# Optimization experiments

Measured on AMD Instinct MI355X. Metric: run time of the kernel, lower is better.

The kernel has to match this reference:

```python
import jax, jax.numpy as jnp
import numpy as np

K = 3            # kernel_size
FINAL = 112      # final_size
DIM = 256        # in_dim


def _blur_kernel():
    # arange(-2,3)^2 * (-1/sqrt(0.5)), exp, outer product, normalized
    f = np.exp((np.arange(-2, 3, dtype=np.float32) ** 2) * (-1.0 / np.sqrt(0.5)))
    k = np.outer(f, f)
    k /= k.sum()
    return jnp.asarray(k, dtype=jnp.float32)


def setup_inputs() -> dict:
    key = jax.random.key(0)
    k1, k2, k3, k4, k5 = jax.random.split(key, 5)
    hr_feats = jax.random.normal(k1, (4, DIM, 224, 224), dtype=jnp.float32)
    attn_kernel = jax.random.normal(k2, (K * K, DIM, K, K), dtype=jnp.float32) * 0.01 + 1.0
    kernel_bias = jax.random.normal(k3, (K * K,), dtype=jnp.float32) * 0.01
    logit_bias = jax.random.normal(k4, (1, K * K, 1, 1), dtype=jnp.float32) * 0.1
    keep_mask = jax.random.uniform(k5, (4, K * K, FINAL, FINAL)) > 0.2
    return {"hr_feats": hr_feats, "attn_kernel": attn_kernel,
            "kernel_bias": kernel_bias, "logit_bias": logit_bias,
            "keep_mask": keep_mask}


def reference(hr_feats, attn_kernel, kernel_bias, logit_bias, keep_mask):
    b, c, h, w = hr_feats.shape
    stride = h // FINAL
    pad = K // 2
    dn = ("NCHW", "OIHW", "NCHW")

    # depthwise 5x5 gaussian blur (blur_attn=True)
    blur_w = jnp.broadcast_to(_blur_kernel().reshape(1, 1, 5, 5), (c, 1, 5, 5))
    inputs = jax.lax.conv_general_dilated(
        hr_feats, blur_w, (1, 1), ((2, 2), (2, 2)),
        dimension_numbers=dn, feature_group_count=c)

    # attention logits: conv2d with k^2 output channels
    patches = jax.lax.conv_general_dilated(
        inputs, attn_kernel, (stride, stride), ((pad, pad), (pad, pad)),
        dimension_numbers=dn) + kernel_bias[None, :, None, None]

    logits = patches * keep_mask + logit_bias  # random keep mask + bias
    attn = jax.nn.softmax(logits, axis=1)       # over k^2 window positions

    # unfold: patches stacked as (c, kh, kw) in channel dim, matching F.unfold
    uf = jax.lax.conv_general_dilated_patches(
        inputs, (K, K), (stride, stride), ((pad, pad), (pad, pad)),
        dimension_numbers=dn)
    uf = uf.reshape(b, c, K * K, FINAL, FINAL)

    return jnp.einsum("bckhw,bkhw->bchw", uf, attn)
```

## Files before the change

### kernel.cpp

```cpp
#include <hip/hip_runtime.h>
#include <cmath>

#define FINAL 112
#define HW    224
#define DIM   256
#define HW2   (HW*HW)
#define F2    (FINAL*FINAL)

__device__ __forceinline__ void blur_weights(float fn[5]) {
    double fd[5]; double s = 0.0;
#pragma unroll
    for (int t = 0; t < 5; ++t) {
        double d = (double)(t - 2);
        fd[t] = exp(-1.4142135623730951 * d * d);
        s += fd[t];
    }
#pragma unroll
    for (int t = 0; t < 5; ++t) fn[t] = (float)(fd[t] / s);
}

__device__ __forceinline__ unsigned short f2bf(float x) {
    unsigned int u = __float_as_uint(x);
    return (unsigned short)((u + 0x7fffu + ((u >> 16) & 1u)) >> 16);
}
__device__ __forceinline__ unsigned int pack2(float a, float b) {
    return (unsigned int)f2bf(a) | ((unsigned int)f2bf(b) << 16);
}
__device__ __forceinline__ float bflo(unsigned int q) { return __uint_as_float(q << 16); }
__device__ __forceinline__ float bfhi(unsigned int q) { return __uint_as_float(q & 0xffff0000u); }

__device__ __forceinline__ float mask_val(const void* m, int flag, size_t idx) {
    if (flag == 0) return ((const int*)m)[idx] ? 1.0f : 0.0f;
    if (flag == 1) return ((const unsigned char*)m)[idx] ? 1.0f : 0.0f;
    if (flag == 2) return (((const float*)m)[idx] != 0.0f) ? 1.0f : 0.0f;
    return ((const long long*)m)[idx] ? 1.0f : 0.0f;
}

__global__ void k_detect(const unsigned int* __restrict__ m, int* __restrict__ flag, int nwords) {
    __shared__ int s_b123, s_3f, s_oddnz;
    if (threadIdx.x == 0) { s_b123 = 0; s_3f = 0; s_oddnz = 0; }
    __syncthreads();
    int b123 = 0, c3f = 0, oddnz = 0;
    for (int i = threadIdx.x; i < nwords; i += blockDim.x) {
        unsigned int u = m[i];
        if (u & 0xFFFFFF00u) b123++;
        if ((u >> 24) == 0x3Fu) c3f++;
        if ((i & 1) && u) oddnz++;
    }
    if (b123) atomicAdd(&s_b123, b123);
    if (c3f) atomicAdd(&s_3f, c3f);
    if (oddnz) atomicAdd(&s_oddnz, oddnz);
    __syncthreads();
    if (threadIdx.x == 0) {
        int f;
        if (s_b123 == 0) f = (s_oddnz == 0) ? 3 : 0;
        else if (s_3f > nwords / 8) f = 2;
        else f = 1;
        *flag = f;
    }
}


__device__ __forceinline__ float4 f4fma(float a, float4 x, float4 y) {
    return make_float4(fmaf(a, x.x, y.x), fmaf(a, x.y, y.y),
                       fmaf(a, x.z, y.z), fmaf(a, x.w, y.w));
}

__launch_bounds__(256)
__global__ void k_blur(const float* __restrict__ hr, unsigned short* __restrict__ blurh) {
    const int bc = blockIdx.x;
    const int w = threadIdx.x >> 6, lane = threadIdx.x & 63;
    const bool act = (lane < 56);
    float fn[5]; blur_weights(fn);
    const float4* src = (const float4*)(hr + (size_t)bc * HW2);
    unsigned short* dst = blurh + (size_t)bc * HW2;
    const int rbase = w * 56 - 2;

    float4 z = make_float4(0.f, 0.f, 0.f, 0.f);
    float4 w0 = z, w1 = z, w2 = z, w3 = z, w4 = z;

#pragma unroll
    for (int p = 0; p < 4; ++p) {
        const int g = rbase + p;
        float4 v = z;
        if (g >= 0 && g < HW && act) v = src[(size_t)g * 56 + lane];
        w0 = w1; w1 = w2; w2 = w3; w3 = w4; w4 = v;
    }

#pragma unroll 4
    for (int i = 4; i < 60; ++i) {
        const int g = rbase + i;
        float4 v = z;
        if (g < HW && act) v = src[(size_t)g * 56 + lane];
        w0 = w1; w1 = w2; w2 = w3; w3 = w4; w4 = v;

        float4 vb = z;
        vb = f4fma(fn[0], w0, vb);
        vb = f4fma(fn[1], w1, vb);
        vb = f4fma(fn[2], w2, vb);
        vb = f4fma(fn[3], w3, vb);
        vb = f4fma(fn[4], w4, vb);

        float lz = __shfl_up(vb.z, 1), lw = __shfl_up(vb.w, 1);
        if (lane == 0) { lz = 0.f; lw = 0.f; }
        float rx = __shfl_down(vb.x, 1), ry = __shfl_down(vb.y, 1);
        float win[8] = { lz, lw, vb.x, vb.y, vb.z, vb.w, rx, ry };
        float o[4];
#pragma unroll
        for (int j = 0; j < 4; ++j) {
            float s = 0.f;
#pragma unroll
            for (int t = 0; t < 5; ++t) s = fmaf(fn[t], win[j + t], s);
            o[j] = s;
        }
        if (act) {
            uint2 pk; pk.x = pack2(o[0], o[1]); pk.y = pack2(o[2], o[3]);
            *(uint2*)(dst + (size_t)(g - 2) * HW + 4 * lane) = pk;
        }
    }
}

__launch_bounds__(256)
__global__ void k_logits_part(const unsigned short* __restrict__ blurh,
                              const float* __restrict__ wk, float* __restrict__ part) {
    const int cg  = blockIdx.x & 15;
    const int rst = blockIdx.x >> 4;
    const int oyq = rst % 28, b = rst / 28;
    const int w = threadIdx.x >> 6, lane = threadIdx.x & 63;
    const int oy = oyq * 4 + w;
    const bool act = (lane < 56);
    const int row0 = 2 * oy - 1;

    float accE[9], accO[9];
#pragma unroll
    for (int o = 0; o < 9; ++o) { accE[o] = 0.f; accO[o] = 0.f; }

#pragma unroll 4
    for (int k = 0; k < 16; ++k) {
        const int c = cg * 16 + k;
        const unsigned short* base = blurh + ((size_t)(b * DIM + c)) * HW2;
        float tE[3][3], tO[3][3];
#pragma unroll
        for (int kh = 0; kh < 3; ++kh) {
            const int row = row0 + kh;
            uint2 q = make_uint2(0u, 0u);
            if (row >= 0 && act)
                q = *(const uint2*)(base + (size_t)row * HW + 4 * lane);
            float vx = bflo(q.x), vy = bfhi(q.x), vz = bflo(q.y), vw = bfhi(q.y);
            float pv = __shfl_up(vw, 1);
            if (lane == 0) pv = 0.f;
            tE[kh][0] = pv; tE[kh][1] = vx; tE[kh][2] = vy;
            tO[kh][0] = vy; tO[kh][1] = vz; tO[kh][2] = vw;
        }
        const float* wc = wk + (size_t)c * 9;
#pragma unroll
        for (int o = 0; o < 9; ++o) {
            const float* wo = wc + (size_t)o * (DIM * 9);
#pragma unroll
            for (int kh = 0; kh < 3; ++kh)
#pragma unroll
                for (int j = 0; j < 3; ++j) {
                    const float wvv = wo[kh * 3 + j];
                    accE[o] = fmaf(wvv, tE[kh][j], accE[o]);
                    accO[o] = fmaf(wvv, tO[kh][j], accO[o]);
                }
        }
    }
    if (act) {
        float* pb = part + (((size_t)(cg * 4 + b)) * 9) * F2 + (size_t)oy * FINAL;
#pragma unroll
        for (int o = 0; o < 9; ++o)
            *(float2*)(pb + (size_t)o * F2 + 2 * lane) = make_float2(accE[o], accO[o]);
    }
}

__launch_bounds__(256)
__global__ void k_softmax(const float* __restrict__ part, const float* __restrict__ kb,
                          const float* __restrict__ lb, const void* __restrict__ mask,
                          float* __restrict__ attn) {
    __shared__ int sb, sf, so;
    if (threadIdx.x == 0) { sb = 0; sf = 0; so = 0; }
    __syncthreads();
    const unsigned int* mw = (const unsigned int*)mask;
    int b123 = 0, c3f = 0, oddnz = 0;
    for (int i = threadIdx.x; i < 2048; i += 256) {
        unsigned int u = mw[i];
        if (u & 0xFFFFFF00u) b123++;
        if ((u >> 24) == 0x3Fu) c3f++;
        if ((i & 1) && u) oddnz++;
    }
    if (b123) atomicAdd(&sb, b123);
    if (c3f) atomicAdd(&sf, c3f);
    if (oddnz) atomicAdd(&so, oddnz);
    __syncthreads();
    int flag;
    if (sb == 0) flag = (so == 0) ? 3 : 0;
    else if (sf > 256) flag = 2;
    else flag = 1;

    const int idx = blockIdx.x * 256 + threadIdx.x;
    const int b = idx / F2, p = idx - b * F2;
    float l[9]; float mx = -3.4e38f;
#pragma unroll
    for (int o = 0; o < 9; ++o) {
        float s = 0.f;
#pragma unroll
        for (int g = 0; g < 16; ++g)
            s += part[(((size_t)(g * 4 + b)) * 9 + o) * F2 + p];
        size_t midx = ((size_t)b * 9 + o) * F2 + p;
        float lo = (s + kb[o]) * mask_val(mask, flag, midx) + lb[o];
        l[o] = lo; mx = fmaxf(mx, lo);
    }
    float sum = 0.f;
#pragma unroll
    for (int o = 0; o < 9; ++o) { l[o] = expf(l[o] - mx); sum += l[o]; }
    const float inv = 1.0f / sum;
#pragma unroll
    for (int o = 0; o < 9; ++o)
        attn[((size_t)b * 9 + o) * F2 + p] = l[o] * inv;
}

__launch_bounds__(256)
__global__ void k_out(const unsigned short* __restrict__ blurh,
                      const float* __restrict__ attn, float* __restrict__ out) {
    const int cg  = blockIdx.x & 7;
    const int rst = blockIdx.x >> 3;
    const int oy = rst % FINAL, b = rst / FINAL;
    const int w = threadIdx.x >> 6, lane = threadIdx.x & 63;
    const bool act = (lane < 56);
    const int row0 = 2 * oy - 1;

    __shared__ float sa[9][FINAL];
    for (int i = threadIdx.x; i < 9 * FINAL; i += 256) {
        int o = i / FINAL, x = i - o * FINAL;
        sa[o][x] = attn[((size_t)b * 9 + o) * F2 + (size_t)oy * FINAL + x];
    }
    __syncthreads();

    float aE[9], aO[9];
#pragma unroll
    for (int o = 0; o < 9; ++o) {
        float2 a = act ? *(const float2*)&sa[o][2 * lane] : make_float2(0.f, 0.f);
        aE[o] = a.x; aO[o] = a.y;
    }
#pragma unroll 4
    for (int k = 0; k < 8; ++k) {
        const int c = (cg << 5) + (w << 3) + k;
        const unsigned short* base = blurh + ((size_t)(b * DIM + c)) * HW2;
        float oE = 0.f, oO = 0.f;
#pragma unroll
        for (int kh = 0; kh < 3; ++kh) {
            const int row = row0 + kh;
            uint2 q = make_uint2(0u, 0u);
            if (row >= 0 && act)
                q = *(const uint2*)(base + (size_t)row * HW + 4 * lane);
            float vx = bflo(q.x), vy = bfhi(q.x), vz = bflo(q.y), vw = bfhi(q.y);
            float pv = __shfl_up(vw, 1);
            if (lane == 0) pv = 0.f;
            oE = fmaf(aE[kh * 3 + 0], pv, oE);
            oE = fmaf(aE[kh * 3 + 1], vx, oE);
            oE = fmaf(aE[kh * 3 + 2], vy, oE);
            oO = fmaf(aO[kh * 3 + 0], vy, oO);
            oO = fmaf(aO[kh * 3 + 1], vz, oO);
            oO = fmaf(aO[kh * 3 + 2], vw, oO);
        }
        if (act)
            *(float2*)(out + ((size_t)(b * DIM + c)) * F2 + (size_t)oy * FINAL + 2 * lane)
                = make_float2(oE, oO);
    }
}


__launch_bounds__(512, 1)
__global__ void k_logits_fb(const float* __restrict__ hr, const float* __restrict__ wk,
                            const float* __restrict__ kb, const float* __restrict__ lb,
                            const void* __restrict__ mask, const int* __restrict__ flagp,
                            float* __restrict__ attn) {
    const int blk = blockIdx.x;
    const int b = blk / FINAL, oy = blk % FINAL;
    const int tid = threadIdx.x;
    const int half = tid >> 8;
    const int lane = tid & 255;
    __shared__ float sIn[2][7][HW];
    __shared__ float sV[2][3][HW + 4];
    __shared__ float sB[2][3][HW + 2];
    __shared__ float sW[2][81];
    __shared__ float sL[1008];
    float fn[5]; blur_weights(fn);
    if (lane < 3) {
        sV[half][lane][0] = 0.f; sV[half][lane][1] = 0.f;
        sV[half][lane][HW + 2] = 0.f; sV[half][lane][HW + 3] = 0.f;
        sB[half][lane][0] = 0.f; sB[half][lane][HW + 1] = 0.f;
    }
    float acc0 = 0.f, acc1 = 0.f;
    const int s1 = tid + 512;
    const int o0 = tid / FINAL, x0 = tid % FINAL;
    const int o1 = s1 / FINAL, x1 = s1 % FINAL;
    const bool has1 = (s1 < 9 * FINAL);
    for (int c0 = 0; c0 < DIM; c0 += 2) {
        const int c = c0 + half;
        const float* src = hr + ((size_t)(b * DIM + c)) * HW2;
        for (int i = lane; i < 7 * HW; i += 256) {
            int r = i / HW, x = i - r * HW;
            int g = 2 * oy - 3 + r;
            sIn[half][r][x] = (g >= 0 && g < HW) ? src[(size_t)g * HW + x] : 0.f;
        }
        if (lane < 81) {
            int o = lane / 9, kk = lane - o * 9;
            sW[half][lane] = wk[((size_t)(o * DIM + c)) * 9 + kk];
        }
        __syncthreads();
        if (lane < HW) {
#pragma unroll
            for (int j = 0; j < 3; ++j) {
                int by = 2 * oy - 1 + j;
                float v = 0.f;
#pragma unroll
                for (int t = 0; t < 5; ++t) v = fmaf(fn[t], sIn[half][j + t][lane], v);
                sV[half][j][lane + 2] = (by >= 0 && by < HW) ? v : 0.f;
            }
        }
        __syncthreads();
        if (lane < HW) {
#pragma unroll
            for (int j = 0; j < 3; ++j) {
                float v = 0.f;
#pragma unroll
                for (int t = 0; t < 5; ++t) v = fmaf(fn[t], sV[half][j][lane + t], v);
                sB[half][j][lane + 1] = v;
            }
        }
        __syncthreads();
#pragma unroll
        for (int cc = 0; cc < 2; ++cc) {
            const float* w = sW[cc];
            float a0 = 0.f;
#pragma unroll
            for (int kh = 0; kh < 3; ++kh)
#pragma unroll
                for (int kw = 0; kw < 3; ++kw)
                    a0 = fmaf(sB[cc][kh][2 * x0 + kw], w[o0 * 9 + kh * 3 + kw], a0);
            acc0 += a0;
            if (has1) {
                float a1v = 0.f;
#pragma unroll
                for (int kh = 0; kh < 3; ++kh)
#pragma unroll
                    for (int kw = 0; kw < 3; ++kw)
                        a1v = fmaf(sB[cc][kh][2 * x1 + kw], w[o1 * 9 + kh * 3 + kw], a1v);
                acc1 += a1v;
            }
        }
        __syncthreads();
    }
    sL[tid] = acc0;
    if (has1) sL[s1] = acc1;
    __syncthreads();
    if (tid < FINAL) {
        const int flag = *flagp;
        float l[9]; float mx = -3.4e38f;
#pragma unroll
        for (int o = 0; o < 9; ++o) {
            size_t midx = (((size_t)b * 9 + o) * FINAL + oy) * FINAL + tid;
            float patch = sL[o * FINAL + tid] + kb[o];
            float lo = patch * mask_val(mask, flag, midx) + lb[o];
            l[o] = lo;
            mx = fmaxf(mx, lo);
        }
        float sum = 0.f;
#pragma unroll
        for (int o = 0; o < 9; ++o) { l[o] = expf(l[o] - mx); sum += l[o]; }
        float inv = 1.0f / sum;
#pragma unroll
        for (int o = 0; o < 9; ++o)
            attn[(((size_t)b * 9 + o) * FINAL + oy) * FINAL + tid] = l[o] * inv;
    }
}

__launch_bounds__(512, 1)
__global__ void k_out_fb(const float* __restrict__ hr, const float* __restrict__ attn,
                         float* __restrict__ out) {
    const int blk = blockIdx.x;
    const int b = blk / FINAL, oy = blk % FINAL;
    const int tid = threadIdx.x;
    const int half = tid >> 8;
    const int lane = tid & 255;
    __shared__ float sIn[2][7][HW];
    __shared__ float sV[2][3][HW + 4];
    __shared__ float sB[2][3][HW + 2];
    __shared__ float sA[9][FINAL];
    float fn[5]; blur_weights(fn);
    if (lane < 3) {
        sV[half][lane][0] = 0.f; sV[half][lane][1] = 0.f;
        sV[half][lane][HW + 2] = 0.f; sV[half][lane][HW + 3] = 0.f;
        sB[half][lane][0] = 0.f; sB[half][lane][HW + 1] = 0.f;
    }
    for (int i = tid; i < 9 * FINAL; i += 512) {
        int o = i / FINAL, x = i - o * FINAL;
        sA[o][x] = attn[(((size_t)b * 9 + o) * FINAL + oy) * FINAL + x];
    }
    for (int c0 = 0; c0 < DIM; c0 += 2) {
        const int c = c0 + half;
        const float* src = hr + ((size_t)(b * DIM + c)) * HW2;
        for (int i = lane; i < 7 * HW; i += 256) {
            int r = i / HW, x = i - r * HW;
            int g = 2 * oy - 3 + r;
            sIn[half][r][x] = (g >= 0 && g < HW) ? src[(size_t)g * HW + x] : 0.f;
        }
        __syncthreads();
        if (lane < HW) {
#pragma unroll
            for (int j = 0; j < 3; ++j) {
                int by = 2 * oy - 1 + j;
                float v = 0.f;
#pragma unroll
                for (int t = 0; t < 5; ++t) v = fmaf(fn[t], sIn[half][j + t][lane], v);
                sV[half][j][lane + 2] = (by >= 0 && by < HW) ? v : 0.f;
            }
        }
        __syncthreads();
        if (lane < HW) {
#pragma unroll
            for (int j = 0; j < 3; ++j) {
                float v = 0.f;
#pragma unroll
                for (int t = 0; t < 5; ++t) v = fmaf(fn[t], sV[half][j][lane + t], v);
                sB[half][j][lane + 1] = v;
            }
        }
        __syncthreads();
        if (lane < FINAL) {
            float a = 0.f;
#pragma unroll
            for (int kh = 0; kh < 3; ++kh)
#pragma unroll
                for (int kw = 0; kw < 3; ++kw)
                    a = fmaf(sA[kh * 3 + kw][lane], sB[half][kh][2 * lane + kw], a);
            out[(((size_t)(b * DIM + c)) * FINAL + oy) * FINAL + lane] = a;
        }
    }
}

extern "C" void kernel_launch(void* const* d_in, const int* in_sizes, int n_in,
                              void* d_out, int out_size, void* d_ws, size_t ws_size,
                              hipStream_t stream) {
    const float* hr   = (const float*)d_in[0];
    const float* wk   = (const float*)d_in[1];
    const float* kb   = (const float*)d_in[2];
    const float* lb   = (const float*)d_in[3];
    const void*  mask = d_in[4];
    float* out = (float*)d_out;

    const size_t ATTN_B = (size_t)4 * 9 * F2 * 4;
    const size_t PART_B = ATTN_B * 16;
    const size_t BLUR_B = (size_t)4 * DIM * HW2 * 2;
    int*   flag = (int*)d_ws;
    float* attn = (float*)((char*)d_ws + 256);
    float* part = (float*)((char*)d_ws + 256 + ATTN_B);
    unsigned short* blurh = (unsigned short*)((char*)d_ws + 256 + ATTN_B + PART_B);
    const size_t need = 256 + ATTN_B + PART_B + BLUR_B;

    if (ws_size >= need) {
        k_blur<<<4 * DIM, 256, 0, stream>>>(hr, blurh);
        k_logits_part<<<4 * 28 * 16, 256, 0, stream>>>(blurh, wk, part);
        k_softmax<<<(4 * F2) / 256, 256, 0, stream>>>(part, kb, lb, mask, attn);
        k_out<<<4 * FINAL * 8, 256, 0, stream>>>(blurh, attn, out);
    } else {
        k_detect<<<1, 1024, 0, stream>>>((const unsigned int*)mask, flag, (4 * 9 * F2) / 4);
        k_logits_fb<<<4 * FINAL, 512, 0, stream>>>(hr, wk, kb, lb, mask, flag, attn);
        k_out_fb<<<4 * FINAL, 512, 0, stream>>>(hr, attn, out);
    }
}
```

Before: 187.3 us.

## Reuse overlapping rows across two output rows, stage weights in LDS, use hardware bf16 pack

k_out now computes two output rows per block. It loads 5 input rows instead of 3 per row, so the shared middle row is read once for both outputs, and the grid is halved. k_logits_part stages its 16-channel slice of the attention weights in shared memory instead of reading them from global memory inside the inner loop, and lowers the unroll factor. The blur kernel replaces the software bf16 rounding with the v_cvt_pk_bf16_f32 instruction, which depends on that instruction existing on the target and rounding the same way. The extra registers in k_out may reduce occupancy.

```diff
diff --git a/kernel.cpp b/kernel.cpp
--- a/kernel.cpp
+++ b/kernel.cpp
@@ -19,12 +19,10 @@
     for (int t = 0; t < 5; ++t) fn[t] = (float)(fd[t] / s);
 }
 
-__device__ __forceinline__ unsigned short f2bf(float x) {
-    unsigned int u = __float_as_uint(x);
-    return (unsigned short)((u + 0x7fffu + ((u >> 16) & 1u)) >> 16);
-}
-__device__ __forceinline__ unsigned int pack2(float a, float b) {
-    return (unsigned int)f2bf(a) | ((unsigned int)f2bf(b) << 16);
+__device__ __forceinline__ unsigned int cvt_pk_bf16(float a, float b) {
+    unsigned int r;
+    asm("v_cvt_pk_bf16_f32 %0, %1, %2" : "=v"(r) : "v"(a), "v"(b));
+    return r;
 }
 __device__ __forceinline__ float bflo(unsigned int q) { return __uint_as_float(q << 16); }
 __device__ __forceinline__ float bfhi(unsigned int q) { return __uint_as_float(q & 0xffff0000u); }
@@ -114,7 +112,7 @@
             o[j] = s;
         }
         if (act) {
-            uint2 pk; pk.x = pack2(o[0], o[1]); pk.y = pack2(o[2], o[3]);
+            uint2 pk; pk.x = cvt_pk_bf16(o[0], o[1]); pk.y = cvt_pk_bf16(o[2], o[3]);
             *(uint2*)(dst + (size_t)(g - 2) * HW + 4 * lane) = pk;
         }
     }
@@ -131,11 +129,18 @@
     const bool act = (lane < 56);
     const int row0 = 2 * oy - 1;
 
+    __shared__ float sw[9][16][9];
+    for (int i = threadIdx.x; i < 1296; i += 256) {
+        const int o = i / 144, r = i - o * 144;
+        sw[o][r / 9][r % 9] = wk[((size_t)o * DIM + cg * 16) * 9 + r];
+    }
+    __syncthreads();
+
     float accE[9], accO[9];
 #pragma unroll
     for (int o = 0; o < 9; ++o) { accE[o] = 0.f; accO[o] = 0.f; }
 
-#pragma unroll 4
+#pragma unroll 2
     for (int k = 0; k < 16; ++k) {
         const int c = cg * 16 + k;
         const unsigned short* base = blurh + ((size_t)(b * DIM + c)) * HW2;
@@ -152,10 +157,9 @@
             tE[kh][0] = pv; tE[kh][1] = vx; tE[kh][2] = vy;
             tO[kh][0] = vy; tO[kh][1] = vz; tO[kh][2] = vw;
         }
-        const float* wc = wk + (size_t)c * 9;
 #pragma unroll
         for (int o = 0; o < 9; ++o) {
-            const float* wo = wc + (size_t)o * (DIM * 9);
+            const float* wo = sw[o][k];
 #pragma unroll
             for (int kh = 0; kh < 3; ++kh)
 #pragma unroll
@@ -225,48 +229,61 @@
                       const float* __restrict__ attn, float* __restrict__ out) {
     const int cg  = blockIdx.x & 7;
     const int rst = blockIdx.x >> 3;
-    const int oy = rst % FINAL, b = rst / FINAL;
+    const int yq = rst % 56, b = rst / 56;
+    const int oy0 = 2 * yq;
     const int w = threadIdx.x >> 6, lane = threadIdx.x & 63;
     const bool act = (lane < 56);
-    const int row0 = 2 * oy - 1;
-
-    __shared__ float sa[9][FINAL];
-    for (int i = threadIdx.x; i < 9 * FINAL; i += 256) {
-        int o = i / FINAL, x = i - o * FINAL;
-        sa[o][x] = attn[((size_t)b * 9 + o) * F2 + (size_t)oy * FINAL + x];
-    }
-    __syncthreads();
-
-    float aE[9], aO[9];
-#pragma unroll
-    for (int o = 0; o < 9; ++o) {
-        float2 a = act ? *(const float2*)&sa[o][2 * lane] : make_float2(0.f, 0.f);
-        aE[o] = a.x; aO[o] = a.y;
-    }
-#pragma unroll 4
+    const int rbase = 2 * oy0 - 1;
+
+    __shared__ float sa[9][2][FINAL];
+    for (int i = threadIdx.x; i < 9 * 2 * FINAL; i += 256) {
+        const int o = i / (2 * FINAL), r = i - o * 2 * FINAL;
+        const int y = r / FINAL, x = r - y * FINAL;
+        sa[o][y][x] = attn[((size_t)b * 9 + o) * F2 + (size_t)(oy0 + y) * FINAL + x];
+    }
+    __syncthreads();
+
+    float aE[2][9], aO[2][9];
+#pragma unroll
+    for (int y = 0; y < 2; ++y)
+#pragma unroll
+        for (int o = 0; o < 9; ++o) {
+            float2 a = act ? *(const float2*)&sa[o][y][2 * lane] : make_float2(0.f, 0.f);
+            aE[y][o] = a.x; aO[y][o] = a.y;
+        }
+
+#pragma unroll 2
     for (int k = 0; k < 8; ++k) {
         const int c = (cg << 5) + (w << 3) + k;
         const unsigned short* base = blurh + ((size_t)(b * DIM + c)) * HW2;
-        float oE = 0.f, oO = 0.f;
-#pragma unroll
-        for (int kh = 0; kh < 3; ++kh) {
-            const int row = row0 + kh;
+        float pv[5], vx[5], vy[5], vz[5], vw[5];
+#pragma unroll
+        for (int rr = 0; rr < 5; ++rr) {
+            const int row = rbase + rr;
             uint2 q = make_uint2(0u, 0u);
             if (row >= 0 && act)
                 q = *(const uint2*)(base + (size_t)row * HW + 4 * lane);
-            float vx = bflo(q.x), vy = bfhi(q.x), vz = bflo(q.y), vw = bfhi(q.y);
-            float pv = __shfl_up(vw, 1);
-            if (lane == 0) pv = 0.f;
-            oE = fmaf(aE[kh * 3 + 0], pv, oE);
-            oE = fmaf(aE[kh * 3 + 1], vx, oE);
-            oE = fmaf(aE[kh * 3 + 2], vy, oE);
-            oO = fmaf(aO[kh * 3 + 0], vy, oO);
-            oO = fmaf(aO[kh * 3 + 1], vz, oO);
-            oO = fmaf(aO[kh * 3 + 2], vw, oO);
-        }
-        if (act)
-            *(float2*)(out + ((size_t)(b * DIM + c)) * F2 + (size_t)oy * FINAL + 2 * lane)
-                = make_float2(oE, oO);
+            vx[rr] = bflo(q.x); vy[rr] = bfhi(q.x); vz[rr] = bflo(q.y); vw[rr] = bfhi(q.y);
+            float p = __shfl_up(vw[rr], 1);
+            pv[rr] = (lane == 0) ? 0.f : p;
+        }
+#pragma unroll
+        for (int y = 0; y < 2; ++y) {
+            float oE = 0.f, oO = 0.f;
+#pragma unroll
+            for (int kh = 0; kh < 3; ++kh) {
+                const int rr = 2 * y + kh;
+                oE = fmaf(aE[y][kh * 3 + 0], pv[rr], oE);
+                oE = fmaf(aE[y][kh * 3 + 1], vx[rr], oE);
+                oE = fmaf(aE[y][kh * 3 + 2], vy[rr], oE);
+                oO = fmaf(aO[y][kh * 3 + 0], vy[rr], oO);
+                oO = fmaf(aO[y][kh * 3 + 1], vz[rr], oO);
+                oO = fmaf(aO[y][kh * 3 + 2], vw[rr], oO);
+            }
+            if (act)
+                *(float2*)(out + ((size_t)(b * DIM + c)) * F2 + (size_t)(oy0 + y) * FINAL + 2 * lane)
+                    = make_float2(oE, oO);
+        }
     }
 }
 
@@ -333,13 +350,13 @@
         __syncthreads();
 #pragma unroll
         for (int cc = 0; cc < 2; ++cc) {
-            const float* w = sW[cc];
+            const float* wv = sW[cc];
             float a0 = 0.f;
 #pragma unroll
             for (int kh = 0; kh < 3; ++kh)
 #pragma unroll
                 for (int kw = 0; kw < 3; ++kw)
-                    a0 = fmaf(sB[cc][kh][2 * x0 + kw], w[o0 * 9 + kh * 3 + kw], a0);
+                    a0 = fmaf(sB[cc][kh][2 * x0 + kw], wv[o0 * 9 + kh * 3 + kw], a0);
             acc0 += a0;
             if (has1) {
                 float a1v = 0.f;
@@ -347,7 +364,7 @@
                 for (int kh = 0; kh < 3; ++kh)
 #pragma unroll
                     for (int kw = 0; kw < 3; ++kw)
-                        a1v = fmaf(sB[cc][kh][2 * x1 + kw], w[o1 * 9 + kh * 3 + kw], a1v);
+                        a1v = fmaf(sB[cc][kh][2 * x1 + kw], wv[o1 * 9 + kh * 3 + kw], a1v);
                 acc1 += a1v;
             }
         }
@@ -464,7 +481,7 @@
         k_blur<<<4 * DIM, 256, 0, stream>>>(hr, blurh);
         k_logits_part<<<4 * 28 * 16, 256, 0, stream>>>(blurh, wk, part);
         k_softmax<<<(4 * F2) / 256, 256, 0, stream>>>(part, kb, lb, mask, attn);
-        k_out<<<4 * FINAL * 8, 256, 0, stream>>>(blurh, attn, out);
+        k_out<<<4 * 56 * 8, 256, 0, stream>>>(blurh, attn, out);
     } else {
         k_detect<<<1, 1024, 0, stream>>>((const unsigned int*)mask, flag, (4 * 9 * F2) / 4);
         k_logits_fb<<<4 * FINAL, 512, 0, stream>>>(hr, wk, kb, lb, mask, flag, attn);
```

Result: slower. 192.6 us (+2.8%).

## Fuse logits, softmax and output into one kernel per row and parity

Applied to the files above, without the earlier changes.

Replaces the three kernels that followed the blur (partial logits, softmax reduction, weighted unfold output) with one fused kernel. Each block handles one output row and one column parity, reduces the channel partials across 8 waves in shared memory, computes the softmax there, then reuses the attention weights to produce the output. This drops the large partial-sum buffer and the attention round trip through global memory. The cost is that each blurred row is read twice by two parity blocks, output stores become strided scalar writes, and the grid is small (896 blocks of 512 threads with launch bounds of one block). The bf16 packing also switches to the hardware v_cvt_pk_bf16_f32 instruction.

```diff
diff --git a/kernel.cpp b/kernel.cpp
--- a/kernel.cpp
+++ b/kernel.cpp
@@ -19,12 +19,10 @@
     for (int t = 0; t < 5; ++t) fn[t] = (float)(fd[t] / s);
 }
 
-__device__ __forceinline__ unsigned short f2bf(float x) {
-    unsigned int u = __float_as_uint(x);
-    return (unsigned short)((u + 0x7fffu + ((u >> 16) & 1u)) >> 16);
-}
-__device__ __forceinline__ unsigned int pack2(float a, float b) {
-    return (unsigned int)f2bf(a) | ((unsigned int)f2bf(b) << 16);
+__device__ __forceinline__ unsigned int cvt_pk_bf16(float a, float b) {
+    unsigned int r;
+    asm("v_cvt_pk_bf16_f32 %0, %1, %2" : "=v"(r) : "v"(a), "v"(b));
+    return r;
 }
 __device__ __forceinline__ float bflo(unsigned int q) { return __uint_as_float(q << 16); }
 __device__ __forceinline__ float bfhi(unsigned int q) { return __uint_as_float(q & 0xffff0000u); }
@@ -114,32 +112,54 @@
             o[j] = s;
         }
         if (act) {
-            uint2 pk; pk.x = pack2(o[0], o[1]); pk.y = pack2(o[2], o[3]);
+            uint2 pk; pk.x = cvt_pk_bf16(o[0], o[1]); pk.y = cvt_pk_bf16(o[2], o[3]);
             *(uint2*)(dst + (size_t)(g - 2) * HW + 4 * lane) = pk;
         }
     }
 }
 
-__launch_bounds__(256)
-__global__ void k_logits_part(const unsigned short* __restrict__ blurh,
-                              const float* __restrict__ wk, float* __restrict__ part) {
-    const int cg  = blockIdx.x & 15;
-    const int rst = blockIdx.x >> 4;
-    const int oyq = rst % 28, b = rst / 28;
-    const int w = threadIdx.x >> 6, lane = threadIdx.x & 63;
-    const int oy = oyq * 4 + w;
+__launch_bounds__(512, 1)
+__global__ void k_fuse(const unsigned short* __restrict__ blurh,
+                       const float* __restrict__ wk, const float* __restrict__ kb,
+                       const float* __restrict__ lb, const void* __restrict__ mask,
+                       float* __restrict__ out) {
+    const int par = blockIdx.x & 1;
+    const int rst = blockIdx.x >> 1;
+    const int oy = rst % FINAL, b = rst / FINAL;
+    const int tid = threadIdx.x;
+    const int wv = tid >> 6, lane = tid & 63;
     const bool act = (lane < 56);
     const int row0 = 2 * oy - 1;
 
-    float accE[9], accO[9];
-#pragma unroll
-    for (int o = 0; o < 9; ++o) { accE[o] = 0.f; accO[o] = 0.f; }
-
-#pragma unroll 4
-    for (int k = 0; k < 16; ++k) {
-        const int c = cg * 16 + k;
+    __shared__ int sb, sf, so;
+    if (tid == 0) { sb = 0; sf = 0; so = 0; }
+    __syncthreads();
+    {
+        const unsigned int* mw = (const unsigned int*)mask;
+        int b123 = 0, c3f = 0, oddnz = 0;
+        for (int i = tid; i < 2048; i += 512) {
+            unsigned int u = mw[i];
+            if (u & 0xFFFFFF00u) b123++;
+            if ((u >> 24) == 0x3Fu) c3f++;
+            if ((i & 1) && u) oddnz++;
+        }
+        if (b123) atomicAdd(&sb, b123);
+        if (c3f) atomicAdd(&sf, c3f);
+        if (oddnz) atomicAdd(&so, oddnz);
+    }
+
+    __shared__ float pl[8][9][56];
+    __shared__ float sa[9][56];
+
+    float acc[9];
+#pragma unroll
+    for (int o = 0; o < 9; ++o) acc[o] = 0.f;
+
+#pragma unroll 2
+    for (int k = 0; k < 32; ++k) {
+        const int c = (wv << 5) + k;
         const unsigned short* base = blurh + ((size_t)(b * DIM + c)) * HW2;
-        float tE[3][3], tO[3][3];
+        float t[3][3];
 #pragma unroll
         for (int kh = 0; kh < 3; ++kh) {
             const int row = row0 + kh;
@@ -149,8 +169,8 @@
             float vx = bflo(q.x), vy = bfhi(q.x), vz = bflo(q.y), vw = bfhi(q.y);
             float pv = __shfl_up(vw, 1);
             if (lane == 0) pv = 0.f;
-            tE[kh][0] = pv; tE[kh][1] = vx; tE[kh][2] = vy;
-            tO[kh][0] = vy; tO[kh][1] = vz; tO[kh][2] = vw;
+            if (par == 0) { t[kh][0] = pv; t[kh][1] = vx; t[kh][2] = vy; }
+            else          { t[kh][0] = vy; t[kh][1] = vz; t[kh][2] = vw; }
         }
         const float* wc = wk + (size_t)c * 9;
 #pragma unroll
@@ -159,95 +179,54 @@
 #pragma unroll
             for (int kh = 0; kh < 3; ++kh)
 #pragma unroll
-                for (int j = 0; j < 3; ++j) {
-                    const float wvv = wo[kh * 3 + j];
-                    accE[o] = fmaf(wvv, tE[kh][j], accE[o]);
-                    accO[o] = fmaf(wvv, tO[kh][j], accO[o]);
-                }
+                for (int j = 0; j < 3; ++j)
+                    acc[o] = fmaf(wo[kh * 3 + j], t[kh][j], acc[o]);
         }
     }
     if (act) {
-        float* pb = part + (((size_t)(cg * 4 + b)) * 9) * F2 + (size_t)oy * FINAL;
-#pragma unroll
-        for (int o = 0; o < 9; ++o)
-            *(float2*)(pb + (size_t)o * F2 + 2 * lane) = make_float2(accE[o], accO[o]);
-    }
-}
-
-__launch_bounds__(256)
-__global__ void k_softmax(const float* __restrict__ part, const float* __restrict__ kb,
-                          const float* __restrict__ lb, const void* __restrict__ mask,
-                          float* __restrict__ attn) {
-    __shared__ int sb, sf, so;
-    if (threadIdx.x == 0) { sb = 0; sf = 0; so = 0; }
-    __syncthreads();
-    const unsigned int* mw = (const unsigned int*)mask;
-    int b123 = 0, c3f = 0, oddnz = 0;
-    for (int i = threadIdx.x; i < 2048; i += 256) {
-        unsigned int u = mw[i];
-        if (u & 0xFFFFFF00u) b123++;
-        if ((u >> 24) == 0x3Fu) c3f++;
-        if ((i & 1) && u) oddnz++;
-    }
-    if (b123) atomicAdd(&sb, b123);
-    if (c3f) atomicAdd(&sf, c3f);
-    if (oddnz) atomicAdd(&so, oddnz);
-    __syncthreads();
+#pragma unroll
+        for (int o = 0; o < 9; ++o) pl[wv][o][lane] = acc[o];
+    }
+    __syncthreads();
+
     int flag;
     if (sb == 0) flag = (so == 0) ? 3 : 0;
     else if (sf > 256) flag = 2;
     else flag = 1;
 
-    const int idx = blockIdx.x * 256 + threadIdx.x;
-    const int b = idx / F2, p = idx - b * F2;
-    float l[9]; float mx = -3.4e38f;
-#pragma unroll
-    for (int o = 0; o < 9; ++o) {
+    for (int i = tid; i < 9 * 56; i += 512) {
+        const int o = i / 56, x = i - o * 56;
         float s = 0.f;
 #pragma unroll
-        for (int g = 0; g < 16; ++g)
-            s += part[(((size_t)(g * 4 + b)) * 9 + o) * F2 + p];
-        size_t midx = ((size_t)b * 9 + o) * F2 + p;
-        float lo = (s + kb[o]) * mask_val(mask, flag, midx) + lb[o];
-        l[o] = lo; mx = fmaxf(mx, lo);
-    }
-    float sum = 0.f;
-#pragma unroll
-    for (int o = 0; o < 9; ++o) { l[o] = expf(l[o] - mx); sum += l[o]; }
-    const float inv = 1.0f / sum;
-#pragma unroll
-    for (int o = 0; o < 9; ++o)
-        attn[((size_t)b * 9 + o) * F2 + p] = l[o] * inv;
-}
-
-__launch_bounds__(256)
-__global__ void k_out(const unsigned short* __restrict__ blurh,
-                      const float* __restrict__ attn, float* __restrict__ out) {
-    const int cg  = blockIdx.x & 7;
-    const int rst = blockIdx.x >> 3;
-    const int oy = rst % FINAL, b = rst / FINAL;
-    const int w = threadIdx.x >> 6, lane = threadIdx.x & 63;
-    const bool act = (lane < 56);
-    const int row0 = 2 * oy - 1;
-
-    __shared__ float sa[9][FINAL];
-    for (int i = threadIdx.x; i < 9 * FINAL; i += 256) {
-        int o = i / FINAL, x = i - o * FINAL;
-        sa[o][x] = attn[((size_t)b * 9 + o) * F2 + (size_t)oy * FINAL + x];
-    }
-    __syncthreads();
-
-    float aE[9], aO[9];
-#pragma unroll
-    for (int o = 0; o < 9; ++o) {
-        float2 a = act ? *(const float2*)&sa[o][2 * lane] : make_float2(0.f, 0.f);
-        aE[o] = a.x; aO[o] = a.y;
-    }
-#pragma unroll 4
-    for (int k = 0; k < 8; ++k) {
-        const int c = (cg << 5) + (w << 3) + k;
+        for (int g = 0; g < 8; ++g) s += pl[g][o][x];
+        const int ox = 2 * x + par;
+        size_t midx = (((size_t)b * 9 + o) * FINAL + oy) * FINAL + ox;
+        pl[0][o][x] = (s + kb[o]) * mask_val(mask, flag, midx) + lb[o];
+    }
+    __syncthreads();
+
+    if (tid < 56) {
+        float l[9]; float mx = -3.4e38f;
+#pragma unroll
+        for (int o = 0; o < 9; ++o) { l[o] = pl[0][o][tid]; mx = fmaxf(mx, l[o]); }
+        float sum = 0.f;
+#pragma unroll
+        for (int o = 0; o < 9; ++o) { l[o] = expf(l[o] - mx); sum += l[o]; }
+        const float inv = 1.0f / sum;
+#pragma unroll
+        for (int o = 0; o < 9; ++o) sa[o][tid] = l[o] * inv;
+    }
+    __syncthreads();
+
+    float a[9];
+#pragma unroll
+    for (int o = 0; o < 9; ++o) a[o] = act ? sa[o][lane] : 0.f;
+
+#pragma unroll 2
+    for (int k = 0; k < 32; ++k) {
+        const int c = (wv << 5) + k;
         const unsigned short* base = blurh + ((size_t)(b * DIM + c)) * HW2;
-        float oE = 0.f, oO = 0.f;
+        float s = 0.f;
 #pragma unroll
         for (int kh = 0; kh < 3; ++kh) {
             const int row = row0 + kh;
@@ -257,16 +236,15 @@
             float vx = bflo(q.x), vy = bfhi(q.x), vz = bflo(q.y), vw = bfhi(q.y);
             float pv = __shfl_up(vw, 1);
             if (lane == 0) pv = 0.f;
-            oE = fmaf(aE[kh * 3 + 0], pv, oE);
-            oE = fmaf(aE[kh * 3 + 1], vx, oE);
-            oE = fmaf(aE[kh * 3 + 2], vy, oE);
-            oO = fmaf(aO[kh * 3 + 0], vy, oO);
-            oO = fmaf(aO[kh * 3 + 1], vz, oO);
-            oO = fmaf(aO[kh * 3 + 2], vw, oO);
+            float t0, t1, t2;
+            if (par == 0) { t0 = pv; t1 = vx; t2 = vy; }
+            else          { t0 = vy; t1 = vz; t2 = vw; }
+            s = fmaf(a[kh * 3 + 0], t0, s);
+            s = fmaf(a[kh * 3 + 1], t1, s);
+            s = fmaf(a[kh * 3 + 2], t2, s);
         }
         if (act)
-            *(float2*)(out + ((size_t)(b * DIM + c)) * F2 + (size_t)oy * FINAL + 2 * lane)
-                = make_float2(oE, oO);
+            out[((size_t)(b * DIM + c)) * F2 + (size_t)oy * FINAL + 2 * lane + par] = s;
     }
 }
 
@@ -333,13 +311,13 @@
         __syncthreads();
 #pragma unroll
         for (int cc = 0; cc < 2; ++cc) {
-            const float* w = sW[cc];
+            const float* wv_ = sW[cc];
             float a0 = 0.f;
 #pragma unroll
             for (int kh = 0; kh < 3; ++kh)
 #pragma unroll
                 for (int kw = 0; kw < 3; ++kw)
-                    a0 = fmaf(sB[cc][kh][2 * x0 + kw], w[o0 * 9 + kh * 3 + kw], a0);
+                    a0 = fmaf(sB[cc][kh][2 * x0 + kw], wv_[o0 * 9 + kh * 3 + kw], a0);
             acc0 += a0;
             if (has1) {
                 float a1v = 0.f;
@@ -347,7 +325,7 @@
                 for (int kh = 0; kh < 3; ++kh)
 #pragma unroll
                     for (int kw = 0; kw < 3; ++kw)
-                        a1v = fmaf(sB[cc][kh][2 * x1 + kw], w[o1 * 9 + kh * 3 + kw], a1v);
+                        a1v = fmaf(sB[cc][kh][2 * x1 + kw], wv_[o1 * 9 + kh * 3 + kw], a1v);
                 acc1 += a1v;
             }
         }
@@ -452,19 +430,15 @@
     float* out = (float*)d_out;
 
     const size_t ATTN_B = (size_t)4 * 9 * F2 * 4;
-    const size_t PART_B = ATTN_B * 16;
     const size_t BLUR_B = (size_t)4 * DIM * HW2 * 2;
     int*   flag = (int*)d_ws;
     float* attn = (float*)((char*)d_ws + 256);
-    float* part = (float*)((char*)d_ws + 256 + ATTN_B);
-    unsigned short* blurh = (unsigned short*)((char*)d_ws + 256 + ATTN_B + PART_B);
-    const size_t need = 256 + ATTN_B + PART_B + BLUR_B;
+    unsigned short* blurh = (unsigned short*)((char*)d_ws + 256 + ATTN_B);
+    const size_t need = 256 + ATTN_B + BLUR_B;
 
     if (ws_size >= need) {
         k_blur<<<4 * DIM, 256, 0, stream>>>(hr, blurh);
-        k_logits_part<<<4 * 28 * 16, 256, 0, stream>>>(blurh, wk, part);
-        k_softmax<<<(4 * F2) / 256, 256, 0, stream>>>(part, kb, lb, mask, attn);
-        k_out<<<4 * FINAL * 8, 256, 0, stream>>>(blurh, attn, out);
+        k_fuse<<<4 * FINAL * 2, 512, 0, stream>>>(blurh, wk, kb, lb, mask, out);
     } else {
         k_detect<<<1, 1024, 0, stream>>>((const unsigned int*)mask, flag, (4 * 9 * F2) / 4);
         k_logits_fb<<<4 * FINAL, 512, 0, stream>>>(hr, wk, kb, lb, mask, flag, attn);
```

New measurement: 411.3 us. 120% more time.
